# Kernel optimization log

Measured on AMD Instinct MI355X. Metric: run time of the kernel, lower is better.

The kernel has to match this reference:

```python
import jax, jax.numpy as jnp
import numpy as np

B, N, D_IN, D_MEM, LAYERS = 8, 2048, 128, 128, 3


def setup_inputs() -> dict:
    key = jax.random.key(0)
    k1, k2, k3, k4 = jax.random.split(key, 4)
    inputs = jax.random.normal(k1, (B, N, D_IN), dtype=jnp.float32)
    # attention-derived adjacency: nonnegative weights
    out_adj = jax.random.uniform(k2, (B, N, N), dtype=jnp.float32)
    # per-layer Linear weights (all layers 128->128 here, stacked) with
    # torch nn.Linear-style init scale 1/sqrt(fan_in)
    scale = 1.0 / np.sqrt(D_IN)
    W = jax.random.uniform(k3, (LAYERS, D_IN, D_MEM), minval=-scale, maxval=scale, dtype=jnp.float32)
    b = jax.random.uniform(k4, (LAYERS, D_MEM), minval=-scale, maxval=scale, dtype=jnp.float32)
    return {"inputs": inputs, "out_adj": out_adj, "W": W, "b": b}


def reference(inputs, out_adj, W, b):
    # GCN.forward (eval mode; dropout = identity)
    adj = out_adj  # [B, N, N]
    denom = jnp.sum(adj, axis=2, keepdims=True) + 1.0  # [B, N, 1]
    outputs = inputs  # [B, N, D]
    for l in range(W.shape[0]):
        Ax = jnp.einsum('bij,bjd->bid', adj, outputs)      # aggregate
        AxW = Ax @ W[l] + b[l]                             # per-layer linear
        outputs = jax.nn.relu(AxW / denom)                 # normalize + activate
    return outputs
```

## Files before the change

### kernel.cpp

```cpp
#include <hip/hip_runtime.h>

#define NN 2048
#define DD 128

typedef _Float16 f16x8 __attribute__((ext_vector_type(8)));
typedef float f32x4 __attribute__((ext_vector_type(4)));

__global__ __launch_bounds__(256) void prep_kernel(
    const float* __restrict__ W, _Float16* __restrict__ Wt) {
  int idx = blockIdx.x * 256 + threadIdx.x;
  int l = idx >> 14, r = idx & 16383, d = r >> 7, k = r & 127;
  Wt[idx] = (_Float16)W[l * 16384 + k * 128 + d];
}

__global__ __launch_bounds__(256) void gemmY_kernel(
    const float* __restrict__ X, const _Float16* __restrict__ Wt,
    _Float16* __restrict__ Yt) {
  const int bx = blockIdx.x;
  const int batch = bx & 7, n0 = (bx >> 3) * 32;
  const int tid = threadIdx.x, lane = tid & 63, wave = tid >> 6;
  const int quad = lane >> 4, l15 = lane & 15, d0 = wave * 32;
  const float* Xb = X + (size_t)(batch * NN + n0) * DD;
  f32x4 acc[2][2] = {};
#pragma unroll
  for (int kk = 0; kk < 128; kk += 32) {
    f16x8 a0 = *(const f16x8*)(Wt + (d0 + l15) * DD + kk + quad * 8);
    f16x8 a1 = *(const f16x8*)(Wt + (d0 + 16 + l15) * DD + kk + quad * 8);
#pragma unroll
    for (int fi = 0; fi < 2; ++fi) {
      const float* xp = Xb + (size_t)(fi * 16 + l15) * DD + kk + quad * 8;
      float4 x0 = *(const float4*)xp;
      float4 x1 = *(const float4*)(xp + 4);
      f16x8 b = {(_Float16)x0.x, (_Float16)x0.y, (_Float16)x0.z, (_Float16)x0.w,
                 (_Float16)x1.x, (_Float16)x1.y, (_Float16)x1.z, (_Float16)x1.w};
      acc[0][fi] = __builtin_amdgcn_mfma_f32_16x16x32_f16(a0, b, acc[0][fi], 0, 0, 0);
      acc[1][fi] = __builtin_amdgcn_mfma_f32_16x16x32_f16(a1, b, acc[1][fi], 0, 0, 0);
    }
  }
  _Float16* YtB = Yt + (size_t)batch * DD * NN;
#pragma unroll
  for (int df = 0; df < 2; ++df)
#pragma unroll
    for (int fi = 0; fi < 2; ++fi)
#pragma unroll
      for (int r = 0; r < 4; ++r)
        YtB[(size_t)(d0 + df * 16 + quad * 4 + r) * NN + n0 + fi * 16 + l15] =
            (_Float16)acc[df][fi][r];
}

template<bool LAST>
__global__ __launch_bounds__(256) void agg_kernel(
    const float* __restrict__ adj, const _Float16* __restrict__ Yt,
    const float* __restrict__ bias, const _Float16* __restrict__ Wn,
    _Float16* __restrict__ Ytn, float* __restrict__ out) {
  __shared__ _Float16 Bs[2][32 * 64];
  __shared__ float Xs[32][132];
  __shared__ float bsh[128];
  __shared__ float rd[32];

  const int tid = threadIdx.x, bx = blockIdx.x;
  const int batch = bx & 7, i0 = (bx >> 3) * 32;
  const int lane = tid & 63, wave = tid >> 6;
  const int quad = lane >> 4, l15 = lane & 15, d0 = wave * 32;
  const int ai = tid >> 3, ac = tid & 7;
  const int sc = ac ^ (ai & 7);

  const float* adjR = adj + (size_t)(batch * NN + i0 + ai) * NN + ac * 8;
  const _Float16* YtB = Yt + (size_t)batch * DD * NN;
  const _Float16* Ya0 = YtB + (size_t)(d0 + l15) * NN;
  const _Float16* Ya1 = YtB + (size_t)(d0 + 16 + l15) * NN;

  if (tid < 128) bsh[tid] = bias[tid];

  f32x4 acc[2][2] = {};
  float rowsum = 0.f;

  float4 av0 = *(const float4*)(adjR);
  float4 av1 = *(const float4*)(adjR + 4);
  f16x8 a[2][2];
#pragma unroll
  for (int k2 = 0; k2 < 2; ++k2) {
    a[k2][0] = *(const f16x8*)(Ya0 + k2 * 32 + quad * 8);
    a[k2][1] = *(const f16x8*)(Ya1 + k2 * 32 + quad * 8);
  }

  for (int ko = 0; ko < 32; ++ko) {
    rowsum += ((av0.x + av0.y) + (av0.z + av0.w)) + ((av1.x + av1.y) + (av1.z + av1.w));
    f16x8 h = {(_Float16)av0.x, (_Float16)av0.y, (_Float16)av0.z, (_Float16)av0.w,
               (_Float16)av1.x, (_Float16)av1.y, (_Float16)av1.z, (_Float16)av1.w};
    *(f16x8*)(&Bs[ko & 1][ai * 64 + sc * 8]) = h;
    f16x8 an[2][2];
    if (ko < 31) {
      const int kb = (ko + 1) * 64;
      av0 = *(const float4*)(adjR + kb);
      av1 = *(const float4*)(adjR + kb + 4);
#pragma unroll
      for (int k2 = 0; k2 < 2; ++k2) {
        an[k2][0] = *(const f16x8*)(Ya0 + kb + k2 * 32 + quad * 8);
        an[k2][1] = *(const f16x8*)(Ya1 + kb + k2 * 32 + quad * 8);
      }
    }
    __syncthreads();
    const _Float16* B = Bs[ko & 1];
#pragma unroll
    for (int k2 = 0; k2 < 2; ++k2)
#pragma unroll
      for (int fi = 0; fi < 2; ++fi) {
        const int row = fi * 16 + l15;
        const int ch = (k2 * 4 + quad) ^ (row & 7);
        f16x8 b = *(const f16x8*)(&B[row * 64 + ch * 8]);
        acc[0][fi] = __builtin_amdgcn_mfma_f32_16x16x32_f16(a[k2][0], b, acc[0][fi], 0, 0, 0);
        acc[1][fi] = __builtin_amdgcn_mfma_f32_16x16x32_f16(a[k2][1], b, acc[1][fi], 0, 0, 0);
      }
#pragma unroll
    for (int k2 = 0; k2 < 2; ++k2) { a[k2][0] = an[k2][0]; a[k2][1] = an[k2][1]; }
  }

  rowsum += __shfl_xor(rowsum, 1);
  rowsum += __shfl_xor(rowsum, 2);
  rowsum += __shfl_xor(rowsum, 4);
  if (ac == 0) rd[ai] = 1.0f / (rowsum + 1.0f);
  __syncthreads();

#pragma unroll
  for (int df = 0; df < 2; ++df)
#pragma unroll
    for (int fi = 0; fi < 2; ++fi)
#pragma unroll
      for (int r = 0; r < 4; ++r) {
        int d = d0 + df * 16 + quad * 4 + r;
        int i = fi * 16 + l15;
        Xs[i][d] = fmaxf((acc[df][fi][r] + bsh[d]) * rd[i], 0.f);
      }
  __syncthreads();

  if (LAST) {
    float* outB = out + (size_t)(batch * NN + i0) * DD;
#pragma unroll
    for (int u = 0; u < 4; ++u) {
      int c = tid + 256 * u;
      int i = c >> 5, f4 = (c & 31) * 4;
      *(float4*)(outB + (size_t)i * DD + f4) = *(const float4*)&Xs[i][f4];
    }
  } else {
    f32x4 acc2[2][2] = {};
#pragma unroll
    for (int kk = 0; kk < 128; kk += 32) {
      f16x8 a0 = *(const f16x8*)(Wn + (d0 + l15) * DD + kk + quad * 8);
      f16x8 a1 = *(const f16x8*)(Wn + (d0 + 16 + l15) * DD + kk + quad * 8);
#pragma unroll
      for (int fi = 0; fi < 2; ++fi) {
        const float* xp = &Xs[fi * 16 + l15][kk + quad * 8];
        f16x8 b = {(_Float16)xp[0], (_Float16)xp[1], (_Float16)xp[2], (_Float16)xp[3],
                   (_Float16)xp[4], (_Float16)xp[5], (_Float16)xp[6], (_Float16)xp[7]};
        acc2[0][fi] = __builtin_amdgcn_mfma_f32_16x16x32_f16(a0, b, acc2[0][fi], 0, 0, 0);
        acc2[1][fi] = __builtin_amdgcn_mfma_f32_16x16x32_f16(a1, b, acc2[1][fi], 0, 0, 0);
      }
    }
    _Float16* YnB = Ytn + (size_t)batch * DD * NN;
#pragma unroll
    for (int df = 0; df < 2; ++df)
#pragma unroll
      for (int fi = 0; fi < 2; ++fi)
#pragma unroll
        for (int r = 0; r < 4; ++r)
          YnB[(size_t)(d0 + df * 16 + quad * 4 + r) * NN + i0 + fi * 16 + l15] =
              (_Float16)acc2[df][fi][r];
  }
}

extern "C" void kernel_launch(void* const* d_in, const int* in_sizes, int n_in,
                              void* d_out, int out_size, void* d_ws, size_t ws_size,
                              hipStream_t stream) {
  const float* x0   = (const float*)d_in[0];
  const float* adj  = (const float*)d_in[1];
  const float* W    = (const float*)d_in[2];
  const float* bias = (const float*)d_in[3];
  float* out = (float*)d_out;

  _Float16* Wt   = (_Float16*)d_ws;
  _Float16* YtA  = (_Float16*)((char*)d_ws + 131072);
  _Float16* YtB_ = (_Float16*)d_out;

  dim3 blk(256);
  prep_kernel <<<192, blk, 0, stream>>>(W, Wt);
  gemmY_kernel<<<512, blk, 0, stream>>>(x0, Wt, YtA);
  agg_kernel<false><<<512, blk, 0, stream>>>(adj, YtA,  bias,       Wt + 16384, YtB_, nullptr);
  agg_kernel<false><<<512, blk, 0, stream>>>(adj, YtB_, bias + 128, Wt + 32768, YtA,  nullptr);
  agg_kernel<true ><<<512, blk, 0, stream>>>(adj, YtA,  bias + 256, nullptr,    nullptr, out);
}
```

Baseline: 290.8 us.

## Cache fp16 adjacency and row norms after first layer, drop LDS staging

The first aggregation pass converts the fp32 adjacency to fp16 and writes it, along with the row-sum reciprocals, to workspace. Later layers read the half-size fp16 copy and the stored reciprocals. Adjacency fragments are loaded directly into registers with double buffering instead of being staged through shared memory with barriers. The per-layer weight GEMM becomes a separate kernel. The aggregation grid is split over output-feature halves with 128-thread blocks, which duplicates adjacency reads across the two halves and adds launches and an extra write of adjacency.

Result: slower. 412.3 us (+41.8%).

```diff
diff --git a/kernel.cpp b/kernel.cpp
--- a/kernel.cpp
+++ b/kernel.cpp
@@ -13,14 +13,14 @@
   Wt[idx] = (_Float16)W[l * 16384 + k * 128 + d];
 }
 
+template<bool F32IN>
 __global__ __launch_bounds__(256) void gemmY_kernel(
-    const float* __restrict__ X, const _Float16* __restrict__ Wt,
+    const void* __restrict__ Xin, const _Float16* __restrict__ Wt,
     _Float16* __restrict__ Yt) {
   const int bx = blockIdx.x;
   const int batch = bx & 7, n0 = (bx >> 3) * 32;
   const int tid = threadIdx.x, lane = tid & 63, wave = tid >> 6;
   const int quad = lane >> 4, l15 = lane & 15, d0 = wave * 32;
-  const float* Xb = X + (size_t)(batch * NN + n0) * DD;
   f32x4 acc[2][2] = {};
 #pragma unroll
   for (int kk = 0; kk < 128; kk += 32) {
@@ -28,11 +28,18 @@
     f16x8 a1 = *(const f16x8*)(Wt + (d0 + 16 + l15) * DD + kk + quad * 8);
 #pragma unroll
     for (int fi = 0; fi < 2; ++fi) {
-      const float* xp = Xb + (size_t)(fi * 16 + l15) * DD + kk + quad * 8;
-      float4 x0 = *(const float4*)xp;
-      float4 x1 = *(const float4*)(xp + 4);
-      f16x8 b = {(_Float16)x0.x, (_Float16)x0.y, (_Float16)x0.z, (_Float16)x0.w,
-                 (_Float16)x1.x, (_Float16)x1.y, (_Float16)x1.z, (_Float16)x1.w};
+      f16x8 b;
+      if (F32IN) {
+        const float* xp = (const float*)Xin +
+            (size_t)(batch * NN + n0 + fi * 16 + l15) * DD + kk + quad * 8;
+        float4 x0 = *(const float4*)xp;
+        float4 x1 = *(const float4*)(xp + 4);
+        b = f16x8{(_Float16)x0.x, (_Float16)x0.y, (_Float16)x0.z, (_Float16)x0.w,
+                  (_Float16)x1.x, (_Float16)x1.y, (_Float16)x1.z, (_Float16)x1.w};
+      } else {
+        b = *(const f16x8*)((const _Float16*)Xin +
+            (size_t)(batch * NN + n0 + fi * 16 + l15) * DD + kk + quad * 8);
+      }
       acc[0][fi] = __builtin_amdgcn_mfma_f32_16x16x32_f16(a0, b, acc[0][fi], 0, 0, 0);
       acc[1][fi] = __builtin_amdgcn_mfma_f32_16x16x32_f16(a1, b, acc[1][fi], 0, 0, 0);
     }
@@ -48,124 +55,134 @@
             (_Float16)acc[df][fi][r];
 }
 
-template<bool LAST>
-__global__ __launch_bounds__(256) void agg_kernel(
-    const float* __restrict__ adj, const _Float16* __restrict__ Yt,
-    const float* __restrict__ bias, const _Float16* __restrict__ Wn,
-    _Float16* __restrict__ Ytn, float* __restrict__ out) {
-  __shared__ _Float16 Bs[2][32 * 64];
-  __shared__ float Xs[32][132];
-  __shared__ float bsh[128];
-  __shared__ float rd[32];
+template<bool FIRST, bool LAST>
+__global__ __launch_bounds__(128) void agg_kernel(
+    const float* __restrict__ adj, _Float16* __restrict__ adjh,
+    const _Float16* __restrict__ Yt, const float* __restrict__ bias,
+    float* __restrict__ rdg, _Float16* __restrict__ act,
+    float* __restrict__ out) {
+  __shared__ __align__(16) char smem[32 * 68 * 4];
+  float    (*Xf)[68] = (float(*)[68])smem;
+  _Float16 (*Xh)[72] = (_Float16(*)[72])smem;
 
   const int tid = threadIdx.x, bx = blockIdx.x;
-  const int batch = bx & 7, i0 = (bx >> 3) * 32;
-  const int lane = tid & 63, wave = tid >> 6;
-  const int quad = lane >> 4, l15 = lane & 15, d0 = wave * 32;
-  const int ai = tid >> 3, ac = tid & 7;
-  const int sc = ac ^ (ai & 7);
-
-  const float* adjR = adj + (size_t)(batch * NN + i0 + ai) * NN + ac * 8;
-  const _Float16* YtB = Yt + (size_t)batch * DD * NN;
-  const _Float16* Ya0 = YtB + (size_t)(d0 + l15) * NN;
-  const _Float16* Ya1 = YtB + (size_t)(d0 + 16 + l15) * NN;
-
-  if (tid < 128) bsh[tid] = bias[tid];
+  const int batch = bx & 7;
+  const int idx = bx >> 3;
+  const int i0 = (idx >> 1) * 32;
+  const int dB = (idx & 1) * 64;
+  const int lane = tid & 63, dh = tid >> 6;
+  const int quad = lane >> 4, l15 = lane & 15;
+
+  const float*    bp0 = adj  + (size_t)(batch * NN + i0 + l15) * NN + quad * 8;
+  const float*    bp1 = bp0 + (size_t)16 * NN;
+  _Float16*       sp0 = adjh + (size_t)(batch * NN + i0 + l15) * NN + quad * 8;
+  _Float16*       sp1 = sp0 + (size_t)16 * NN;
+  const _Float16* hp0 = adjh + (size_t)(batch * NN + i0 + l15) * NN + quad * 8;
+  const _Float16* hp1 = hp0 + (size_t)16 * NN;
+  const _Float16* ap0 = Yt + (size_t)batch * DD * NN +
+                        (size_t)(dB + dh * 32 + l15) * NN + quad * 8;
+  const _Float16* ap1 = ap0 + (size_t)16 * NN;
+  const bool storeAdj = FIRST && (idx & 1) == 0 && dh == 0;
 
   f32x4 acc[2][2] = {};
-  float rowsum = 0.f;
-
-  float4 av0 = *(const float4*)(adjR);
-  float4 av1 = *(const float4*)(adjR + 4);
+  float rs0 = 0.f, rs1 = 0.f;
+
   f16x8 a[2][2];
-#pragma unroll
-  for (int k2 = 0; k2 < 2; ++k2) {
-    a[k2][0] = *(const f16x8*)(Ya0 + k2 * 32 + quad * 8);
-    a[k2][1] = *(const f16x8*)(Ya1 + k2 * 32 + quad * 8);
-  }
-
-  for (int ko = 0; ko < 32; ++ko) {
-    rowsum += ((av0.x + av0.y) + (av0.z + av0.w)) + ((av1.x + av1.y) + (av1.z + av1.w));
-    f16x8 h = {(_Float16)av0.x, (_Float16)av0.y, (_Float16)av0.z, (_Float16)av0.w,
-               (_Float16)av1.x, (_Float16)av1.y, (_Float16)av1.z, (_Float16)av1.w};
-    *(f16x8*)(&Bs[ko & 1][ai * 64 + sc * 8]) = h;
-    f16x8 an[2][2];
-    if (ko < 31) {
-      const int kb = (ko + 1) * 64;
-      av0 = *(const float4*)(adjR + kb);
-      av1 = *(const float4*)(adjR + kb + 4);
-#pragma unroll
-      for (int k2 = 0; k2 < 2; ++k2) {
-        an[k2][0] = *(const f16x8*)(Ya0 + kb + k2 * 32 + quad * 8);
-        an[k2][1] = *(const f16x8*)(Ya1 + kb + k2 * 32 + quad * 8);
+  float4 bf[2][2][2];
+  f16x8 bh[2][2];
+
+#define LDB(ks, buf)                                            \
+  do {                                                          \
+    if (FIRST) {                                                \
+      bf[buf][0][0] = *(const float4*)(bp0 + (ks));             \
+      bf[buf][0][1] = *(const float4*)(bp0 + (ks) + 4);         \
+      bf[buf][1][0] = *(const float4*)(bp1 + (ks));             \
+      bf[buf][1][1] = *(const float4*)(bp1 + (ks) + 4);         \
+    } else {                                                    \
+      bh[buf][0] = *(const f16x8*)(hp0 + (ks));                 \
+      bh[buf][1] = *(const f16x8*)(hp1 + (ks));                 \
+    }                                                           \
+    a[buf][0] = *(const f16x8*)(ap0 + (ks));                    \
+    a[buf][1] = *(const f16x8*)(ap1 + (ks));                    \
+  } while (0)
+
+  LDB(0, 0);
+  LDB(32, 1);
+
+#pragma unroll 4
+  for (int s = 0; s < 64; ++s) {
+    const int buf = s & 1;
+    f16x8 b0, b1;
+    if (FIRST) {
+      float4 x0 = bf[buf][0][0], x1 = bf[buf][0][1];
+      float4 y0 = bf[buf][1][0], y1 = bf[buf][1][1];
+      rs0 += ((x0.x + x0.y) + (x0.z + x0.w)) + ((x1.x + x1.y) + (x1.z + x1.w));
+      rs1 += ((y0.x + y0.y) + (y0.z + y0.w)) + ((y1.x + y1.y) + (y1.z + y1.w));
+      b0 = f16x8{(_Float16)x0.x, (_Float16)x0.y, (_Float16)x0.z, (_Float16)x0.w,
+                 (_Float16)x1.x, (_Float16)x1.y, (_Float16)x1.z, (_Float16)x1.w};
+      b1 = f16x8{(_Float16)y0.x, (_Float16)y0.y, (_Float16)y0.z, (_Float16)y0.w,
+                 (_Float16)y1.x, (_Float16)y1.y, (_Float16)y1.z, (_Float16)y1.w};
+      if (storeAdj) {
+        *(f16x8*)(sp0 + s * 32) = b0;
+        *(f16x8*)(sp1 + s * 32) = b1;
       }
-    }
-    __syncthreads();
-    const _Float16* B = Bs[ko & 1];
-#pragma unroll
-    for (int k2 = 0; k2 < 2; ++k2)
-#pragma unroll
-      for (int fi = 0; fi < 2; ++fi) {
-        const int row = fi * 16 + l15;
-        const int ch = (k2 * 4 + quad) ^ (row & 7);
-        f16x8 b = *(const f16x8*)(&B[row * 64 + ch * 8]);
-        acc[0][fi] = __builtin_amdgcn_mfma_f32_16x16x32_f16(a[k2][0], b, acc[0][fi], 0, 0, 0);
-        acc[1][fi] = __builtin_amdgcn_mfma_f32_16x16x32_f16(a[k2][1], b, acc[1][fi], 0, 0, 0);
-      }
-#pragma unroll
-    for (int k2 = 0; k2 < 2; ++k2) { a[k2][0] = an[k2][0]; a[k2][1] = an[k2][1]; }
-  }
-
-  rowsum += __shfl_xor(rowsum, 1);
-  rowsum += __shfl_xor(rowsum, 2);
-  rowsum += __shfl_xor(rowsum, 4);
-  if (ac == 0) rd[ai] = 1.0f / (rowsum + 1.0f);
+    } else {
+      b0 = bh[buf][0];
+      b1 = bh[buf][1];
+    }
+    f16x8 a0c = a[buf][0], a1c = a[buf][1];
+    if (s < 62) LDB((s + 2) * 32, buf);
+    acc[0][0] = __builtin_amdgcn_mfma_f32_16x16x32_f16(a0c, b0, acc[0][0], 0, 0, 0);
+    acc[0][1] = __builtin_amdgcn_mfma_f32_16x16x32_f16(a0c, b1, acc[0][1], 0, 0, 0);
+    acc[1][0] = __builtin_amdgcn_mfma_f32_16x16x32_f16(a1c, b0, acc[1][0], 0, 0, 0);
+    acc[1][1] = __builtin_amdgcn_mfma_f32_16x16x32_f16(a1c, b1, acc[1][1], 0, 0, 0);
+  }
+#undef LDB
+
+  float rdv0, rdv1;
+  if (FIRST) {
+    rs0 += __shfl_xor(rs0, 16); rs0 += __shfl_xor(rs0, 32);
+    rs1 += __shfl_xor(rs1, 16); rs1 += __shfl_xor(rs1, 32);
+    rdv0 = 1.0f / (rs0 + 1.0f);
+    rdv1 = 1.0f / (rs1 + 1.0f);
+    if (storeAdj && quad == 0) {
+      rdg[batch * NN + i0 + l15] = rdv0;
+      rdg[batch * NN + i0 + 16 + l15] = rdv1;
+    }
+  } else {
+    rdv0 = rdg[batch * NN + i0 + l15];
+    rdv1 = rdg[batch * NN + i0 + 16 + l15];
+  }
+
+#pragma unroll
+  for (int af = 0; af < 2; ++af)
+#pragma unroll
+    for (int r = 0; r < 4; ++r) {
+      int dl = dh * 32 + af * 16 + quad * 4 + r;
+      float bv = bias[dB + dl];
+      float v0 = fmaxf((acc[af][0][r] + bv) * rdv0, 0.f);
+      float v1 = fmaxf((acc[af][1][r] + bv) * rdv1, 0.f);
+      if (LAST) { Xf[l15][dl] = v0;            Xf[16 + l15][dl] = v1; }
+      else      { Xh[l15][dl] = (_Float16)v0;  Xh[16 + l15][dl] = (_Float16)v1; }
+    }
   __syncthreads();
 
-#pragma unroll
-  for (int df = 0; df < 2; ++df)
-#pragma unroll
-    for (int fi = 0; fi < 2; ++fi)
-#pragma unroll
-      for (int r = 0; r < 4; ++r) {
-        int d = d0 + df * 16 + quad * 4 + r;
-        int i = fi * 16 + l15;
-        Xs[i][d] = fmaxf((acc[df][fi][r] + bsh[d]) * rd[i], 0.f);
-      }
-  __syncthreads();
-
   if (LAST) {
-    float* outB = out + (size_t)(batch * NN + i0) * DD;
+    float* ob = out + (size_t)(batch * NN + i0) * DD + dB;
 #pragma unroll
     for (int u = 0; u < 4; ++u) {
-      int c = tid + 256 * u;
-      int i = c >> 5, f4 = (c & 31) * 4;
-      *(float4*)(outB + (size_t)i * DD + f4) = *(const float4*)&Xs[i][f4];
+      int c = tid + 128 * u;
+      int i = c >> 4, f4 = (c & 15) * 4;
+      *(float4*)(ob + (size_t)i * DD + f4) = *(const float4*)&Xf[i][f4];
     }
   } else {
-    f32x4 acc2[2][2] = {};
-#pragma unroll
-    for (int kk = 0; kk < 128; kk += 32) {
-      f16x8 a0 = *(const f16x8*)(Wn + (d0 + l15) * DD + kk + quad * 8);
-      f16x8 a1 = *(const f16x8*)(Wn + (d0 + 16 + l15) * DD + kk + quad * 8);
-#pragma unroll
-      for (int fi = 0; fi < 2; ++fi) {
-        const float* xp = &Xs[fi * 16 + l15][kk + quad * 8];
-        f16x8 b = {(_Float16)xp[0], (_Float16)xp[1], (_Float16)xp[2], (_Float16)xp[3],
-                   (_Float16)xp[4], (_Float16)xp[5], (_Float16)xp[6], (_Float16)xp[7]};
-        acc2[0][fi] = __builtin_amdgcn_mfma_f32_16x16x32_f16(a0, b, acc2[0][fi], 0, 0, 0);
-        acc2[1][fi] = __builtin_amdgcn_mfma_f32_16x16x32_f16(a1, b, acc2[1][fi], 0, 0, 0);
-      }
-    }
-    _Float16* YnB = Ytn + (size_t)batch * DD * NN;
-#pragma unroll
-    for (int df = 0; df < 2; ++df)
-#pragma unroll
-      for (int fi = 0; fi < 2; ++fi)
-#pragma unroll
-        for (int r = 0; r < 4; ++r)
-          YnB[(size_t)(d0 + df * 16 + quad * 4 + r) * NN + i0 + fi * 16 + l15] =
-              (_Float16)acc2[df][fi][r];
+    _Float16* ab = act + (size_t)(batch * NN + i0) * DD + dB;
+#pragma unroll
+    for (int u = 0; u < 2; ++u) {
+      int c = tid + 128 * u;
+      int i = c >> 3, h = (c & 7) * 8;
+      *(uint4*)(ab + (size_t)i * DD + h) = *(const uint4*)&Xh[i][h];
+    }
   }
 }
 
@@ -178,14 +195,20 @@
   const float* bias = (const float*)d_in[3];
   float* out = (float*)d_out;
 
-  _Float16* Wt   = (_Float16*)d_ws;
-  _Float16* YtA  = (_Float16*)((char*)d_ws + 131072);
-  _Float16* YtB_ = (_Float16*)d_out;
-
-  dim3 blk(256);
-  prep_kernel <<<192, blk, 0, stream>>>(W, Wt);
-  gemmY_kernel<<<512, blk, 0, stream>>>(x0, Wt, YtA);
-  agg_kernel<false><<<512, blk, 0, stream>>>(adj, YtA,  bias,       Wt + 16384, YtB_, nullptr);
-  agg_kernel<false><<<512, blk, 0, stream>>>(adj, YtB_, bias + 128, Wt + 32768, YtA,  nullptr);
-  agg_kernel<true ><<<512, blk, 0, stream>>>(adj, YtA,  bias + 256, nullptr,    nullptr, out);
-}
+  char* ws = (char*)d_ws;
+  _Float16* Wt   = (_Float16*)ws;
+  float*    rdg  = (float*)(ws + (1u << 17));
+  _Float16* YtA  = (_Float16*)(ws + (1u << 20));
+  _Float16* YtB  = (_Float16*)(ws + 6u * (1u << 20));
+  _Float16* actA = (_Float16*)(ws + 11u * (1u << 20));
+  _Float16* actB = (_Float16*)(ws + 16u * (1u << 20));
+  _Float16* adjh = (_Float16*)(ws + 32u * (1u << 20));
+
+  prep_kernel        <<<192, 256, 0, stream>>>(W, Wt);
+  gemmY_kernel<true> <<<512, 256, 0, stream>>>(x0, Wt, YtA);
+  agg_kernel<true , false><<<1024, 128, 0, stream>>>(adj, adjh, YtA, bias,       rdg, actA, nullptr);
+  gemmY_kernel<false><<<512, 256, 0, stream>>>(actA, Wt + 16384, YtB);
+  agg_kernel<false, false><<<1024, 128, 0, stream>>>(adj, adjh, YtB, bias + 128, rdg, actB, nullptr);
+  gemmY_kernel<false><<<512, 256, 0, stream>>>(actB, Wt + 32768, YtA);
+  agg_kernel<false, true ><<<1024, 128, 0, stream>>>(adj, adjh, YtA, bias + 256, rdg, nullptr, out);
+}
```

## Stream adjacency tiles straight into LDS via global_load_lds with larger K tile

Applied to the files above, without the earlier changes.

The aggregation kernel now copies fp32 adjacency tiles directly from global memory into shared memory with the asynchronous global_load_lds path, double-buffered, and the K tile grows from 64 to 128. Conversion to fp16 and the row-sum reduction move to the consumer side, after the tile is read from LDS. This is meant to remove the register round-trip and per-thread conversion stores on the producer side and to halve the number of barriers. In exchange it doubles LDS use, since tiles are held as fp32, and it repeats the fp32-to-fp16 conversion in every wave that reads a tile. The ping-pong Y buffers also move from the output buffer into the workspace.

Result: slower. 513.5 us (+76.6%).

```diff
diff --git a/kernel.cpp b/kernel.cpp
--- a/kernel.cpp
+++ b/kernel.cpp
@@ -2,6 +2,8 @@
 
 #define NN 2048
 #define DD 128
+#define BK 128
+#define NT (NN / BK)
 
 typedef _Float16 f16x8 __attribute__((ext_vector_type(8)));
 typedef float f32x4 __attribute__((ext_vector_type(4)));
@@ -20,7 +22,6 @@
   const int batch = bx & 7, n0 = (bx >> 3) * 32;
   const int tid = threadIdx.x, lane = tid & 63, wave = tid >> 6;
   const int quad = lane >> 4, l15 = lane & 15, d0 = wave * 32;
-  const float* Xb = X + (size_t)(batch * NN + n0) * DD;
   f32x4 acc[2][2] = {};
 #pragma unroll
   for (int kk = 0; kk < 128; kk += 32) {
@@ -28,7 +29,7 @@
     f16x8 a1 = *(const f16x8*)(Wt + (d0 + 16 + l15) * DD + kk + quad * 8);
 #pragma unroll
     for (int fi = 0; fi < 2; ++fi) {
-      const float* xp = Xb + (size_t)(fi * 16 + l15) * DD + kk + quad * 8;
+      const float* xp = X + (size_t)(batch * NN + n0 + fi * 16 + l15) * DD + kk + quad * 8;
       float4 x0 = *(const float4*)xp;
       float4 x1 = *(const float4*)(xp + 4);
       f16x8 b = {(_Float16)x0.x, (_Float16)x0.y, (_Float16)x0.z, (_Float16)x0.w,
@@ -53,94 +54,98 @@
     const float* __restrict__ adj, const _Float16* __restrict__ Yt,
     const float* __restrict__ bias, const _Float16* __restrict__ Wn,
     _Float16* __restrict__ Ytn, float* __restrict__ out) {
-  __shared__ _Float16 Bs[2][32 * 64];
-  __shared__ float Xs[32][132];
+  __shared__ __align__(16) float Bsm[2][32 * BK];
+  __shared__ __align__(16) float acts[32][132];
   __shared__ float bsh[128];
-  __shared__ float rd[32];
 
   const int tid = threadIdx.x, bx = blockIdx.x;
   const int batch = bx & 7, i0 = (bx >> 3) * 32;
-  const int lane = tid & 63, wave = tid >> 6;
-  const int quad = lane >> 4, l15 = lane & 15, d0 = wave * 32;
-  const int ai = tid >> 3, ac = tid & 7;
-  const int sc = ac ^ (ai & 7);
+  const int wave = tid >> 6, lane = tid & 63;
+  const int quad = lane >> 4, l15 = lane & 15;
+  const int d0 = wave * 32;
+  const int l31 = lane & 31, lh = lane >> 5;
 
-  const float* adjR = adj + (size_t)(batch * NN + i0 + ai) * NN + ac * 8;
-  const _Float16* YtB = Yt + (size_t)batch * DD * NN;
-  const _Float16* Ya0 = YtB + (size_t)(d0 + l15) * NN;
-  const _Float16* Ya1 = YtB + (size_t)(d0 + 16 + l15) * NN;
+  const float* adjB = adj + (size_t)(batch * NN + i0) * NN;
+  const _Float16* YA0 = Yt + (size_t)batch * DD * NN + (size_t)(d0 + l15) * NN + quad * 8;
+  const _Float16* YA1 = YA0 + (size_t)16 * NN;
 
   if (tid < 128) bsh[tid] = bias[tid];
 
   f32x4 acc[2][2] = {};
-  float rowsum = 0.f;
+  float rs0 = 0.f, rs1 = 0.f;
+  f16x8 a[2][4][2];
 
-  float4 av0 = *(const float4*)(adjR);
-  float4 av1 = *(const float4*)(adjR + 4);
-  f16x8 a[2][2];
+  auto STAGE = [&](int ko, int buf) {
 #pragma unroll
-  for (int k2 = 0; k2 < 2; ++k2) {
-    a[k2][0] = *(const f16x8*)(Ya0 + k2 * 32 + quad * 8);
-    a[k2][1] = *(const f16x8*)(Ya1 + k2 * 32 + quad * 8);
-  }
+    for (int u = 0; u < 4; ++u) {
+      const int rt = wave * 8 + u * 2 + lh;
+      const float* g = adjB + (size_t)rt * NN + ko * BK + ((l31 ^ (rt & 7)) << 2);
+      __builtin_amdgcn_global_load_lds(
+          (const __attribute__((address_space(1))) unsigned int*)g,
+          (__attribute__((address_space(3))) unsigned int*)
+              &Bsm[buf][(wave * 8 + u * 2) * BK],
+          16, 0, 0);
+    }
+  };
+  auto LOADA = [&](int ko, int buf) {
+#pragma unroll
+    for (int kk = 0; kk < 4; ++kk) {
+      a[buf][kk][0] = *(const f16x8*)(YA0 + ko * BK + kk * 32);
+      a[buf][kk][1] = *(const f16x8*)(YA1 + ko * BK + kk * 32);
+    }
+  };
 
-  for (int ko = 0; ko < 32; ++ko) {
-    rowsum += ((av0.x + av0.y) + (av0.z + av0.w)) + ((av1.x + av1.y) + (av1.z + av1.w));
-    f16x8 h = {(_Float16)av0.x, (_Float16)av0.y, (_Float16)av0.z, (_Float16)av0.w,
-               (_Float16)av1.x, (_Float16)av1.y, (_Float16)av1.z, (_Float16)av1.w};
-    *(f16x8*)(&Bs[ko & 1][ai * 64 + sc * 8]) = h;
-    f16x8 an[2][2];
-    if (ko < 31) {
-      const int kb = (ko + 1) * 64;
-      av0 = *(const float4*)(adjR + kb);
-      av1 = *(const float4*)(adjR + kb + 4);
+  STAGE(0, 0);
+  LOADA(0, 0);
+  __syncthreads();
+
+  for (int ko = 0; ko < NT; ++ko) {
+    const int buf = ko & 1;
+    if (ko + 1 < NT) { STAGE(ko + 1, buf ^ 1); LOADA(ko + 1, buf ^ 1); }
+    const float* Bt = Bsm[buf];
 #pragma unroll
-      for (int k2 = 0; k2 < 2; ++k2) {
-        an[k2][0] = *(const f16x8*)(Ya0 + kb + k2 * 32 + quad * 8);
-        an[k2][1] = *(const f16x8*)(Ya1 + kb + k2 * 32 + quad * 8);
+    for (int kk = 0; kk < 4; ++kk) {
+#pragma unroll
+      for (int fi = 0; fi < 2; ++fi) {
+        const int row = fi * 16 + l15;
+        const int c0 = kk * 8 + quad * 2;
+        const float* rp = Bt + row * BK;
+        float4 w0 = *(const float4*)(rp + ((c0 ^ (row & 7)) << 2));
+        float4 w1 = *(const float4*)(rp + (((c0 + 1) ^ (row & 7)) << 2));
+        float s = ((w0.x + w0.y) + (w0.z + w0.w)) + ((w1.x + w1.y) + (w1.z + w1.w));
+        if (fi == 0) rs0 += s; else rs1 += s;
+        f16x8 b = {(_Float16)w0.x, (_Float16)w0.y, (_Float16)w0.z, (_Float16)w0.w,
+                   (_Float16)w1.x, (_Float16)w1.y, (_Float16)w1.z, (_Float16)w1.w};
+        acc[0][fi] = __builtin_amdgcn_mfma_f32_16x16x32_f16(a[buf][kk][0], b, acc[0][fi], 0, 0, 0);
+        acc[1][fi] = __builtin_amdgcn_mfma_f32_16x16x32_f16(a[buf][kk][1], b, acc[1][fi], 0, 0, 0);
       }
     }
     __syncthreads();
-    const _Float16* B = Bs[ko & 1];
-#pragma unroll
-    for (int k2 = 0; k2 < 2; ++k2)
-#pragma unroll
-      for (int fi = 0; fi < 2; ++fi) {
-        const int row = fi * 16 + l15;
-        const int ch = (k2 * 4 + quad) ^ (row & 7);
-        f16x8 b = *(const f16x8*)(&B[row * 64 + ch * 8]);
-        acc[0][fi] = __builtin_amdgcn_mfma_f32_16x16x32_f16(a[k2][0], b, acc[0][fi], 0, 0, 0);
-        acc[1][fi] = __builtin_amdgcn_mfma_f32_16x16x32_f16(a[k2][1], b, acc[1][fi], 0, 0, 0);
-      }
-#pragma unroll
-    for (int k2 = 0; k2 < 2; ++k2) { a[k2][0] = an[k2][0]; a[k2][1] = an[k2][1]; }
   }
 
-  rowsum += __shfl_xor(rowsum, 1);
-  rowsum += __shfl_xor(rowsum, 2);
-  rowsum += __shfl_xor(rowsum, 4);
-  if (ac == 0) rd[ai] = 1.0f / (rowsum + 1.0f);
-  __syncthreads();
+  rs0 += __shfl_xor(rs0, 16); rs0 += __shfl_xor(rs0, 32);
+  rs1 += __shfl_xor(rs1, 16); rs1 += __shfl_xor(rs1, 32);
+  const float rdv0 = 1.0f / (rs0 + 1.0f);
+  const float rdv1 = 1.0f / (rs1 + 1.0f);
 
 #pragma unroll
-  for (int df = 0; df < 2; ++df)
+  for (int af = 0; af < 2; ++af)
 #pragma unroll
-    for (int fi = 0; fi < 2; ++fi)
-#pragma unroll
-      for (int r = 0; r < 4; ++r) {
-        int d = d0 + df * 16 + quad * 4 + r;
-        int i = fi * 16 + l15;
-        Xs[i][d] = fmaxf((acc[df][fi][r] + bsh[d]) * rd[i], 0.f);
-      }
+    for (int r = 0; r < 4; ++r) {
+      const int d = d0 + af * 16 + quad * 4 + r;
+      const float bv = bsh[d];
+      acts[l15][d]      = fmaxf((acc[af][0][r] + bv) * rdv0, 0.f);
+      acts[16 + l15][d] = fmaxf((acc[af][1][r] + bv) * rdv1, 0.f);
+    }
   __syncthreads();
 
   if (LAST) {
-    float* outB = out + (size_t)(batch * NN + i0) * DD;
+    float* ob = out + (size_t)(batch * NN + i0) * DD;
 #pragma unroll
     for (int u = 0; u < 4; ++u) {
       int c = tid + 256 * u;
       int i = c >> 5, f4 = (c & 31) * 4;
-      *(float4*)(outB + (size_t)i * DD + f4) = *(const float4*)&Xs[i][f4];
+      *(float4*)(ob + (size_t)i * DD + f4) = *(const float4*)&acts[i][f4];
     }
   } else {
     f32x4 acc2[2][2] = {};
@@ -150,22 +155,24 @@
       f16x8 a1 = *(const f16x8*)(Wn + (d0 + 16 + l15) * DD + kk + quad * 8);
 #pragma unroll
       for (int fi = 0; fi < 2; ++fi) {
-        const float* xp = &Xs[fi * 16 + l15][kk + quad * 8];
-        f16x8 b = {(_Float16)xp[0], (_Float16)xp[1], (_Float16)xp[2], (_Float16)xp[3],
-                   (_Float16)xp[4], (_Float16)xp[5], (_Float16)xp[6], (_Float16)xp[7]};
+        const float* xp = &acts[fi * 16 + l15][kk + quad * 8];
+        float4 x0 = *(const float4*)xp;
+        float4 x1 = *(const float4*)(xp + 4);
+        f16x8 b = {(_Float16)x0.x, (_Float16)x0.y, (_Float16)x0.z, (_Float16)x0.w,
+                   (_Float16)x1.x, (_Float16)x1.y, (_Float16)x1.z, (_Float16)x1.w};
         acc2[0][fi] = __builtin_amdgcn_mfma_f32_16x16x32_f16(a0, b, acc2[0][fi], 0, 0, 0);
         acc2[1][fi] = __builtin_amdgcn_mfma_f32_16x16x32_f16(a1, b, acc2[1][fi], 0, 0, 0);
       }
     }
     _Float16* YnB = Ytn + (size_t)batch * DD * NN;
 #pragma unroll
-    for (int df = 0; df < 2; ++df)
+    for (int af = 0; af < 2; ++af)
 #pragma unroll
       for (int fi = 0; fi < 2; ++fi)
 #pragma unroll
         for (int r = 0; r < 4; ++r)
-          YnB[(size_t)(d0 + df * 16 + quad * 4 + r) * NN + i0 + fi * 16 + l15] =
-              (_Float16)acc2[df][fi][r];
+          YnB[(size_t)(d0 + af * 16 + quad * 4 + r) * NN + i0 + fi * 16 + l15] =
+              (_Float16)acc2[af][fi][r];
   }
 }
 
@@ -178,14 +185,14 @@
   const float* bias = (const float*)d_in[3];
   float* out = (float*)d_out;
 
-  _Float16* Wt   = (_Float16*)d_ws;
-  _Float16* YtA  = (_Float16*)((char*)d_ws + 131072);
-  _Float16* YtB_ = (_Float16*)d_out;
+  char* ws = (char*)d_ws;
+  _Float16* Wt  = (_Float16*)ws;
+  _Float16* Yt0 = (_Float16*)(ws + (1u << 20));
+  _Float16* Yt1 = (_Float16*)(ws + 6u * (1u << 20));
 
-  dim3 blk(256);
-  prep_kernel <<<192, blk, 0, stream>>>(W, Wt);
-  gemmY_kernel<<<512, blk, 0, stream>>>(x0, Wt, YtA);
-  agg_kernel<false><<<512, blk, 0, stream>>>(adj, YtA,  bias,       Wt + 16384, YtB_, nullptr);
-  agg_kernel<false><<<512, blk, 0, stream>>>(adj, YtB_, bias + 128, Wt + 32768, YtA,  nullptr);
-  agg_kernel<true ><<<512, blk, 0, stream>>>(adj, YtA,  bias + 256, nullptr,    nullptr, out);
+  prep_kernel <<<192, 256, 0, stream>>>(W, Wt);
+  gemmY_kernel<<<512, 256, 0, stream>>>(x0, Wt, Yt0);
+  agg_kernel<false><<<512, 256, 0, stream>>>(adj, Yt0, bias,       Wt + 16384, Yt1, nullptr);
+  agg_kernel<false><<<512, 256, 0, stream>>>(adj, Yt1, bias + 128, Wt + 32768, Yt0, nullptr);
+  agg_kernel<true ><<<512, 256, 0, stream>>>(adj, Yt0, bias + 256, nullptr,    nullptr, out);
 }
```
